# Kernel optimization log

Measured on AMD Instinct MI355X. Metric: run time of the kernel, lower is better.

The kernel has to match this reference:

```python
import jax, jax.numpy as jnp
import numpy as np

DIM = 512
HEADS = 8
DIM_HEAD = 64
INNER = HEADS * DIM_HEAD  # 512
NARROW_K = 9
WIDE_K = 9
WIDE_DIL = 5


def setup_inputs() -> dict:
    key = jax.random.key(0)
    ks = jax.random.split(key, 12)
    b, n = 4, 2048
    s = lambda fan_in: 1.0 / np.sqrt(fan_in)
    inp = {
        'tokens': jax.random.normal(ks[0], (b, n, DIM), jnp.float32),
        'mask': jax.random.randint(ks[1], (b, n), 0, 2) > 0,
        'w_qkv': jax.random.normal(ks[2], (DIM, INNER * 3), jnp.float32) * s(DIM),
        'w_out': jax.random.normal(ks[3], (INNER, DIM), jnp.float32) * s(INNER),
        'b_out': jnp.zeros((DIM,), jnp.float32),
        'w_narrow': jax.random.normal(ks[4], (DIM, DIM, NARROW_K), jnp.float32) * s(DIM * NARROW_K),
        'b_narrow': jnp.zeros((DIM,), jnp.float32),
        'w_wide': jax.random.normal(ks[5], (DIM, DIM, WIDE_K), jnp.float32) * s(DIM * WIDE_K),
        'b_wide': jnp.zeros((DIM,), jnp.float32),
        'ln1_g': jnp.ones((DIM,), jnp.float32),
        'ln1_b': jnp.zeros((DIM,), jnp.float32),
        'ff_w': jax.random.normal(ks[6], (DIM, DIM), jnp.float32) * s(DIM),
        'ff_b': jnp.zeros((DIM,), jnp.float32),
        'ln2_g': jnp.ones((DIM,), jnp.float32),
        'ln2_b': jnp.zeros((DIM,), jnp.float32),
    }
    return inp


def layer_norm(x, g, b, eps=1e-5):
    m = jnp.mean(x, axis=-1, keepdims=True)
    v = jnp.mean(jnp.square(x - m), axis=-1, keepdims=True)
    return (x - m) / jnp.sqrt(v + eps) * g + b


def rope_encoding(seq_len, dim_head, dtype):
    inv_freq = 1.0 / (10000.0 ** (jnp.arange(0, dim_head, 2, dtype=jnp.float32) / dim_head))
    pos = jnp.arange(seq_len, dtype=jnp.float32)
    sinu = jnp.einsum('i,j->ij', pos, inv_freq)  # [n, d/2]
    return jnp.concatenate([jnp.sin(sinu), jnp.cos(sinu)], axis=-1).astype(dtype)  # [n, d]


def attn(tokens, mask, w_qkv, w_out, b_out):
    b, n, _ = tokens.shape
    qkv = tokens @ w_qkv  # [b, n, 3*inner]
    q, k, v = jnp.split(qkv, 3, axis=-1)
    reshp = lambda t: t.reshape(b, n, HEADS, DIM_HEAD).transpose(0, 2, 1, 3)  # b h n d
    q, k, v = reshp(q), reshp(k), reshp(v)
    rope = rope_encoding(n, DIM_HEAD, tokens.dtype)  # [n, d]
    q = q + rope
    k = k + rope
    mask4 = mask[:, None, :, None]  # b 1 n 1
    big = jnp.finfo(k.dtype).max
    k = jnp.where(mask4, k, -big)
    q = jax.nn.softmax(q, axis=-1) * (DIM_HEAD ** -0.5)
    k = jax.nn.softmax(k, axis=2)  # over n
    v = jnp.where(mask4, v, 0.0)
    context = jnp.einsum('bhnd,bhne->bhde', k, v)
    out = jnp.einsum('bhde,bhnd->bhne', context, q)
    out = out.transpose(0, 2, 1, 3).reshape(b, n, INNER)
    return out @ w_out + b_out


def conv1d(x, w, b, padding, dilation):
    # x: [b, c, n], w: [out, in, k]
    y = jax.lax.conv_general_dilated(
        x, w, window_strides=(1,), padding=[(padding, padding)],
        rhs_dilation=(dilation,), dimension_numbers=('NCW', 'OIW', 'NCW'))
    return y + b[None, :, None]


def reference(tokens, mask, w_qkv, w_out, b_out, w_narrow, b_narrow,
              w_wide, b_wide, ln1_g, ln1_b, ff_w, ff_b, ln2_g, ln2_b):
    tokens = attn(tokens, mask, w_qkv, w_out, b_out)
    conv_in = tokens.transpose(0, 2, 1)  # b d n
    conv_in = jnp.where(mask[:, None, :], conv_in, 0.0)
    narrow = jax.nn.gelu(conv1d(conv_in, w_narrow, b_narrow, NARROW_K // 2, 1), approximate=False)
    wide_pad = (WIDE_K + (WIDE_K - 1) * (WIDE_DIL - 1)) // 2  # 20
    wide = jax.nn.gelu(conv1d(conv_in, w_wide, b_wide, wide_pad, WIDE_DIL), approximate=False)
    tokens = tokens + narrow.transpose(0, 2, 1) + wide.transpose(0, 2, 1)
    tokens = layer_norm(tokens, ln1_g, ln1_b)
    tokens = layer_norm(jax.nn.gelu(tokens @ ff_w + ff_b, approximate=False), ln2_g, ln2_b)
    return tokens
```

## Files before the change

### kernel.cpp

```cpp
#include <hip/hip_runtime.h>
#include <hip/hip_bf16.h>

#define BB 4
#define NN 2048
#define NROWS (BB*NN)

typedef unsigned short u16;
typedef __bf16 bf16x8 __attribute__((ext_vector_type(8)));
typedef u16    u16x8  __attribute__((ext_vector_type(8)));
typedef float  fx4    __attribute__((ext_vector_type(4)));

__device__ __forceinline__ float bf2f(u16 u){
  union { float f; unsigned int i; } x; x.i = ((unsigned int)u) << 16; return x.f;
}
__device__ __forceinline__ u16 f2bf(float f){
  union { float f; unsigned int i; } x; x.f = f;
  unsigned int i = x.i;
  i += 0x7fffu + ((i >> 16) & 1u);
  return (u16)(i >> 16);
}
__device__ __forceinline__ float geluf(float x){
  return 0.5f * x * (1.0f + erff(x * 0.70710678118654752f));
}

__global__ __launch_bounds__(256) void sniff_k(const u16* tokens, const unsigned int* mask, int* flags){
  __shared__ int s_f32, s_byte;
  if (threadIdx.x == 0) { s_f32 = 0; s_byte = 0; }
  __syncthreads();
  for (int i = threadIdx.x; i < 4096; i += 256) {
    float v = bf2f(tokens[i]);
    if (!(fabsf(v) < 1e10f)) atomicOr(&s_f32, 1);
  }
  for (int i = threadIdx.x; i < 2048; i += 256) {
    if (mask[i] > 1u) atomicOr(&s_byte, 1);
  }
  __syncthreads();
  if (threadIdx.x == 0) { flags[0] = s_f32; flags[1] = s_byte; }
}

__global__ __launch_bounds__(256) void misc_k(const void* mask, const void* tokens,
                                              const void* p0, const void* p1, const void* p2,
                                              const void* p3, const void* p4, const void* p5,
                                              const void* p6, const void* p7,
                                              const int* flags, float* rope, int* m32,
                                              float* params, float* ctx, float* kS, u16* tokbf){
  const void* srcs[8] = {p0,p1,p2,p3,p4,p5,p6,p7};
  int f32 = flags[0], mbyte = flags[1];
  const int T = 131072 + 8192 + 4096 + 131072 + 2048 + 4194304;
  for (int i = blockIdx.x*256 + threadIdx.x; i < T; i += gridDim.x*256) {
    if (i < 131072) {
      int p = i >> 6, j = i & 63;
      int jj = (j < 32) ? j : j - 32;
      float invf = exp2f(-(float)jj * (13.287712379549449f/32.0f));
      float prod = (float)p * invf;
      rope[i] = (j < 32) ? sinf(prod) : cosf(prod);
    } else if (i < 139264) {
      int k = i - 131072;
      int v = mbyte ? (int)((const unsigned char*)mask)[k] : ((const int*)mask)[k];
      m32[k] = v ? 1 : 0;
    } else if (i < 143360) {
      int k = i - 139264;
      int pid = k >> 9, j = k & 511;
      const void* s = srcs[pid];
      params[k] = f32 ? ((const float*)s)[j] : bf2f(((const u16*)s)[j]);
    } else if (i < 274432) {
      ctx[i - 143360] = 0.0f;
    } else if (i < 276480) {
      kS[i - 274432] = 0.0f;
    } else {
      int k = i - 276480;
      tokbf[k] = f32 ? f2bf(((const float*)tokens)[k]) : ((const u16*)tokens)[k];
    }
  }
}

__global__ __launch_bounds__(256) void prep2_k(const void* w_qkv, const void* w_out, const void* ff_w,
                                               const void* w_narrow, const void* w_wide,
                                               const int* flags,
                                               u16* wqkvt, u16* woutt, u16* ffwt,
                                               u16* wtN2, u16* wtW2){
  int bid = blockIdx.x;
  int f = flags[0];
  int tid = threadIdx.x;
  if (bid < 1024) {
    int tensor = bid >> 9, o = bid & 511;
    const void* src = tensor ? w_wide : w_narrow;
    u16* dst = tensor ? wtW2 : wtN2;
    __shared__ u16 Ls[4608];
    for (int i = tid; i < 4608; i += 256) {
      Ls[i] = f ? f2bf(((const float*)src)[(size_t)o*4608 + i]) : ((const u16*)src)[(size_t)o*4608 + i];
    }
    __syncthreads();
    #pragma unroll
    for (int kk = 0; kk < 9; kk++) {
      #pragma unroll
      for (int u = 0; u < 2; u++) {
        int c = tid + u*256;
        dst[(size_t)kk*262144 + o*512 + c] = Ls[c*9 + kk];
      }
    }
  } else {
    int id = bid - 1024;
    int z = id / 192;
    int rem = id - z*192;
    int x = rem % 24, y = rem / 24;
    int Nn = (z == 0) ? 1536 : 512;
    if (x * 64 >= Nn) return;
    const void* src = (z == 0) ? w_qkv : (z == 1) ? w_out : ff_w;
    u16* dst = (z == 0) ? wqkvt : (z == 1) ? woutt : ffwt;
    __shared__ u16 Ts[64][72];
    int n0 = x * 64, k0 = y * 64;
    int r = tid >> 2, cq = (tid & 3) * 16;
    #pragma unroll
    for (int u = 0; u < 2; u++) {
      int c = cq + u*8;
      int sidx = (k0 + r)*Nn + n0 + c;
      u16x8 v;
      if (f) {
        #pragma unroll
        for (int j = 0; j < 8; j++) v[j] = f2bf(((const float*)src)[sidx + j]);
      } else {
        v = *(const u16x8*)&((const u16*)src)[sidx];
      }
      *(u16x8*)&Ts[r][c] = v;
    }
    __syncthreads();
    #pragma unroll
    for (int u = 0; u < 2; u++) {
      int c = cq + u*8;
      u16x8 v;
      #pragma unroll
      for (int j = 0; j < 8; j++) v[j] = Ts[c + j][r];
      *(u16x8*)&dst[(size_t)(n0 + r)*512 + k0 + c] = v;
    }
  }
}

__global__ __launch_bounds__(256) void mgemm_qkv_k(const u16* A, const u16* Bt, const float* rope,
                                                   const int* mask, u16* qb, u16* keb, u16* vb){
  __shared__ u16 As[128][40];
  __shared__ u16 Bs[128][40];
  __shared__ int smask[128];
  int tid = threadIdx.x;
  int lane = tid & 63;
  int wave = tid >> 6;
  int wm = (wave >> 1) * 64, wn = (wave & 1) * 64;
  int quad = lane >> 4, l16 = lane & 15;
  int m0 = blockIdx.y * 128, n0 = blockIdx.x * 128;
  fx4 acc[4][4] = {};
  int ar = tid >> 2;
  int ac = (tid & 3) * 8;
  for (int k0 = 0; k0 < 512; k0 += 32) {
    *(u16x8*)&As[ar][ac]    = *(const u16x8*)&A[(size_t)(m0+ar)*512 + k0 + ac];
    *(u16x8*)&As[ar+64][ac] = *(const u16x8*)&A[(size_t)(m0+ar+64)*512 + k0 + ac];
    *(u16x8*)&Bs[ar][ac]    = *(const u16x8*)&Bt[(size_t)(n0+ar)*512 + k0 + ac];
    *(u16x8*)&Bs[ar+64][ac] = *(const u16x8*)&Bt[(size_t)(n0+ar+64)*512 + k0 + ac];
    __syncthreads();
    bf16x8 af[4], bfv[4];
    #pragma unroll
    for (int i = 0; i < 4; i++)
      af[i] = __builtin_bit_cast(bf16x8, *(const u16x8*)&As[wm + i*16 + l16][quad*8]);
    #pragma unroll
    for (int j = 0; j < 4; j++)
      bfv[j] = __builtin_bit_cast(bf16x8, *(const u16x8*)&Bs[wn + j*16 + l16][quad*8]);
    #pragma unroll
    for (int i = 0; i < 4; i++)
      #pragma unroll
      for (int j = 0; j < 4; j++)
        acc[i][j] = __builtin_amdgcn_mfma_f32_16x16x32_bf16(af[i], bfv[j], acc[i][j], 0, 0, 0);
    __syncthreads();
  }
  int x = blockIdx.x;
  if (x >= 4) {
    if (tid < 128) smask[tid] = mask[m0 + tid];
    __syncthreads();
  }
  if (x < 4) {
    #pragma unroll
    for (int i = 0; i < 4; i++)
      #pragma unroll
      for (int r = 0; r < 4; r++) {
        int rl = wm + i*16 + quad*4 + r;
        int row = m0 + rl;
        int nseq = row & (NN-1);
        const float* rp = rope + nseq*64 + l16;
        float e0 = __expf(acc[i][0][r] + rp[0]);
        float e1 = __expf(acc[i][1][r] + rp[16]);
        float e2 = __expf(acc[i][2][r] + rp[32]);
        float e3 = __expf(acc[i][3][r] + rp[48]);
        float s = e0 + e1 + e2 + e3;
        s += __shfl_xor(s, 1); s += __shfl_xor(s, 2);
        s += __shfl_xor(s, 4); s += __shfl_xor(s, 8);
        float sc = 0.125f / s;
        size_t base = (size_t)row*512 + n0 + wn + l16;
        qb[base]      = f2bf(e0*sc);
        qb[base + 16] = f2bf(e1*sc);
        qb[base + 32] = f2bf(e2*sc);
        qb[base + 48] = f2bf(e3*sc);
      }
  } else if (x < 8) {
    #pragma unroll
    for (int i = 0; i < 4; i++)
      #pragma unroll
      for (int r = 0; r < 4; r++) {
        int rl = wm + i*16 + quad*4 + r;
        int row = m0 + rl;
        int nseq = row & (NN-1);
        int mk = smask[rl];
        const float* rp = rope + nseq*64 + l16;
        size_t base = (size_t)row*512 + (n0 - 512) + wn + l16;
        #pragma unroll
        for (int j = 0; j < 4; j++) {
          float ke = mk ? __expf(acc[i][j][r] + rp[j*16]) : 0.0f;
          keb[base + j*16] = f2bf(ke);
        }
      }
  } else {
    #pragma unroll
    for (int i = 0; i < 4; i++)
      #pragma unroll
      for (int r = 0; r < 4; r++) {
        int rl = wm + i*16 + quad*4 + r;
        int row = m0 + rl;
        int mk = smask[rl];
        size_t base = (size_t)row*512 + (n0 - 1024) + wn + l16;
        #pragma unroll
        for (int j = 0; j < 4; j++)
          vb[base + j*16] = mk ? f2bf(acc[i][j][r]) : (u16)0;
      }
  }
}

#define FMA16(a, b, acc) \
  acc[0][0] = fmaf(a.x, b.x, acc[0][0]); acc[0][1] = fmaf(a.x, b.y, acc[0][1]); \
  acc[0][2] = fmaf(a.x, b.z, acc[0][2]); acc[0][3] = fmaf(a.x, b.w, acc[0][3]); \
  acc[1][0] = fmaf(a.y, b.x, acc[1][0]); acc[1][1] = fmaf(a.y, b.y, acc[1][1]); \
  acc[1][2] = fmaf(a.y, b.z, acc[1][2]); acc[1][3] = fmaf(a.y, b.w, acc[1][3]); \
  acc[2][0] = fmaf(a.z, b.x, acc[2][0]); acc[2][1] = fmaf(a.z, b.y, acc[2][1]); \
  acc[2][2] = fmaf(a.z, b.z, acc[2][2]); acc[2][3] = fmaf(a.z, b.w, acc[2][3]); \
  acc[3][0] = fmaf(a.w, b.x, acc[3][0]); acc[3][1] = fmaf(a.w, b.y, acc[3][1]); \
  acc[3][2] = fmaf(a.w, b.z, acc[3][2]); acc[3][3] = fmaf(a.w, b.w, acc[3][3]);

__global__ __launch_bounds__(256) void ctx_k(const u16* keb, const u16* vb, float* ctx, float* Sg){
  int bh = blockIdx.x, seg = blockIdx.y;
  int b = bh >> 3, h = bh & 7;
  __shared__ float Ks[32][68], Vs[32][68];
  __shared__ float sS[64];
  int tid = threadIdx.x, tx = tid & 15, ty = tid >> 4;
  if (tid < 64) sS[tid] = 0.0f;
  float acc[4][4] = {{0.f,0.f,0.f,0.f},{0.f,0.f,0.f,0.f},{0.f,0.f,0.f,0.f},{0.f,0.f,0.f,0.f}};
  float sp[8] = {0,0,0,0,0,0,0,0};
  int nl = tid >> 3, dcol = (tid & 7)*8;
  const u16* kp0 = keb + (size_t)(b*NN + seg*256)*512 + h*64 + dcol;
  const u16* vp0 = vb  + (size_t)(b*NN + seg*256)*512 + h*64 + dcol;
  for (int nc = 0; nc < 256; nc += 32) {
    u16x8 ku = *(const u16x8*)(kp0 + (size_t)(nc + nl)*512);
    u16x8 vu = *(const u16x8*)(vp0 + (size_t)(nc + nl)*512);
    float a[8], bb[8];
    #pragma unroll
    for (int t = 0; t < 8; t++) { a[t] = bf2f(ku[t]); bb[t] = bf2f(vu[t]); sp[t] += a[t]; }
    *(float4*)&Ks[nl][dcol]   = (float4){a[0],a[1],a[2],a[3]};
    *(float4*)&Ks[nl][dcol+4] = (float4){a[4],a[5],a[6],a[7]};
    *(float4*)&Vs[nl][dcol]   = (float4){bb[0],bb[1],bb[2],bb[3]};
    *(float4*)&Vs[nl][dcol+4] = (float4){bb[4],bb[5],bb[6],bb[7]};
    __syncthreads();
    #pragma unroll
    for (int q = 0; q < 32; q++) {
      float4 a4 = *(const float4*)&Ks[q][ty*4];
      float4 b4 = *(const float4*)&Vs[q][tx*4];
      FMA16(a4, b4, acc)
    }
    __syncthreads();
  }
  #pragma unroll
  for (int j = 0; j < 8; j++) atomicAdd(&sS[dcol + j], sp[j]);
  float* cp = ctx + (size_t)bh*4096;
  #pragma unroll
  for (int i = 0; i < 4; i++)
    #pragma unroll
    for (int j = 0; j < 4; j++)
      atomicAdd(&cp[(ty*4 + i)*64 + tx*4 + j], acc[i][j]);
  __syncthreads();
  if (tid < 64) atomicAdd(&Sg[bh*64 + tid], sS[tid]);
}

__global__ __launch_bounds__(256) void ctxw_k(const float* ctx, const float* Sg, const u16* woutt,
                                              u16* W2t, u16* cpadb){
  int bx = blockIdx.x;
  int tid = threadIdx.x;
  if (bx >= 32) {
    int idx = (bx - 32)*256 + tid;
    if (idx < BB*40*512) {
      int c = idx & 511;
      int t = (idx >> 9) % 40;
      int b = idx / (40*512);
      int tt = (t < 20) ? t : 2048 + t;
      cpadb[((size_t)b*2088 + tt)*512 + c] = 0;
    }
    return;
  }
  int h = bx & 7, b = bx >> 3;
  int lane = tid & 63, wave = tid >> 6;
  int quad = lane >> 4, l16 = lane & 15;
  const float* cp = ctx + (size_t)(b*8 + h)*4096;
  fx4 acc[8][4] = {};
  #pragma unroll
  for (int ks = 0; ks < 2; ks++) {
    bf16x8 bfv[4];
    #pragma unroll
    for (int j = 0; j < 4; j++) {
      int d = j*16 + l16;
      float S = Sg[(b*8 + h)*64 + d];
      float rs = (S > 0.0f) ? 1.0f/S : 0.0f;
      const float* src = cp + d*64 + ks*32 + quad*8;
      float4 v0 = *(const float4*)src, v1 = *(const float4*)(src + 4);
      bf16x8 t;
      t[0]=(__bf16)(v0.x*rs); t[1]=(__bf16)(v0.y*rs); t[2]=(__bf16)(v0.z*rs); t[3]=(__bf16)(v0.w*rs);
      t[4]=(__bf16)(v1.x*rs); t[5]=(__bf16)(v1.y*rs); t[6]=(__bf16)(v1.z*rs); t[7]=(__bf16)(v1.w*rs);
      bfv[j] = t;
    }
    #pragma unroll
    for (int i = 0; i < 8; i++) {
      int orow = wave*128 + i*16 + l16;
      bf16x8 afr = __builtin_bit_cast(bf16x8, *(const u16x8*)&woutt[(size_t)orow*512 + h*64 + ks*32 + quad*8]);
      #pragma unroll
      for (int j = 0; j < 4; j++)
        acc[i][j] = __builtin_amdgcn_mfma_f32_16x16x32_bf16(afr, bfv[j], acc[i][j], 0, 0, 0);
    }
  }
  u16* out = W2t + (size_t)b*262144;
  #pragma unroll
  for (int i = 0; i < 8; i++)
    #pragma unroll
    for (int j = 0; j < 4; j++)
      #pragma unroll
      for (int r = 0; r < 4; r++) {
        int orow = wave*128 + i*16 + quad*4 + r;
        out[(size_t)orow*512 + h*64 + j*16 + l16] = f2bf(acc[i][j][r]);
      }
}

__global__ __launch_bounds__(256) void mgemm_attn64_k(const u16* qb, const u16* W2t, const float* bias,
                                                      const int* mask, u16* attnb, u16* cpadb){
  __shared__ u16 As[64][40];
  __shared__ u16 Bs[128][40];
  int tid = threadIdx.x;
  int lane = tid & 63;
  int wave = tid >> 6;
  int wn = wave * 32;
  int quad = lane >> 4, l16 = lane & 15;
  int m0 = blockIdx.y * 64, n0 = blockIdx.x * 128, b = blockIdx.z;
  const u16* A  = qb  + (size_t)b*2048*512;
  const u16* Bt = W2t + (size_t)b*262144;
  fx4 acc[4][2] = {};
  int ar = tid >> 2;
  int ac = (tid & 3) * 8;
  for (int k0 = 0; k0 < 512; k0 += 32) {
    *(u16x8*)&As[ar][ac]    = *(const u16x8*)&A[(size_t)(m0+ar)*512 + k0 + ac];
    *(u16x8*)&Bs[ar][ac]    = *(const u16x8*)&Bt[(size_t)(n0+ar)*512 + k0 + ac];
    *(u16x8*)&Bs[ar+64][ac] = *(const u16x8*)&Bt[(size_t)(n0+ar+64)*512 + k0 + ac];
    __syncthreads();
    bf16x8 af[4], bfv[2];
    #pragma unroll
    for (int i = 0; i < 4; i++)
      af[i] = __builtin_bit_cast(bf16x8, *(const u16x8*)&As[i*16 + l16][quad*8]);
    #pragma unroll
    for (int j = 0; j < 2; j++)
      bfv[j] = __builtin_bit_cast(bf16x8, *(const u16x8*)&Bs[wn + j*16 + l16][quad*8]);
    #pragma unroll
    for (int i = 0; i < 4; i++)
      #pragma unroll
      for (int j = 0; j < 2; j++)
        acc[i][j] = __builtin_amdgcn_mfma_f32_16x16x32_bf16(af[i], bfv[j], acc[i][j], 0, 0, 0);
    __syncthreads();
  }
  #pragma unroll
  for (int i = 0; i < 4; i++)
    #pragma unroll
    for (int j = 0; j < 2; j++) {
      int col = n0 + wn + j*16 + l16;
      float bv = bias[col];
      #pragma unroll
      for (int r = 0; r < 4; r++) {
        int row_l = m0 + i*16 + quad*4 + r;
        float v = acc[i][j][r] + bv;
        u16 vbb = f2bf(v);
        attnb[((size_t)b*2048 + row_l)*512 + col] = vbb;
        int mk = mask[b*2048 + row_l];
        cpadb[((size_t)b*2088 + row_l + 20)*512 + col] = mk ? vbb : (u16)0;
      }
    }
}

__global__ __launch_bounds__(256, 2) void mconv6_k(const u16* cpad, const u16* Wn, const u16* Ww,
                                                   const float* bias_n, const float* bias_w,
                                                   u16* Dn, u16* Dw){
  __shared__ u16 As[168][72];
  __shared__ u16 Ws[128][72];
  int tid = threadIdx.x;
  int lane = tid & 63;
  int wave = tid >> 6;
  int wm = (wave >> 1) * 64;
  int wo = (wave & 1) * 64;
  int quad = lane >> 4, l16 = lane & 15;
  int o0 = blockIdx.x * 128, m0 = blockIdx.y * 128;
  int b = blockIdx.z >> 1, cid = blockIdx.z & 1;
  const u16* W = cid ? Ww : Wn;
  const float* bias = cid ? bias_w : bias_n;
  u16* D = cid ? Dw : Dn;
  fx4 acc[4][4] = {};
  const u16* cb = cpad + ((size_t)b*2088 + m0)*512;
  for (int c0 = 0; c0 < 512; c0 += 64) {
    __syncthreads();
    for (int idx = tid; idx < 168*8; idx += 256) {
      int r = idx >> 3, off = (idx & 7)*8;
      *(u16x8*)&As[r][off] = *(const u16x8*)&cb[(size_t)r*512 + c0 + off];
    }
    u16x8 pre[4];
    {
      const u16* wp = W + (size_t)o0*512 + c0;
      #pragma unroll
      for (int u = 0; u < 4; u++) {
        int idx = tid + u*256;
        int r = idx >> 3, off = (idx & 7)*8;
        pre[u] = *(const u16x8*)&wp[(size_t)r*512 + off];
      }
    }
    #pragma unroll
    for (int kk = 0; kk < 9; kk++) {
      if (kk > 0) __syncthreads();
      #pragma unroll
      for (int u = 0; u < 4; u++) {
        int idx = tid + u*256;
        int r = idx >> 3, off = (idx & 7)*8;
        *(u16x8*)&Ws[r][off] = pre[u];
      }
      if (kk < 8) {
        const u16* wp = W + (size_t)(kk+1)*262144 + (size_t)o0*512 + c0;
        #pragma unroll
        for (int u = 0; u < 4; u++) {
          int idx = tid + u*256;
          int r = idx >> 3, off = (idx & 7)*8;
          pre[u] = *(const u16x8*)&wp[(size_t)r*512 + off];
        }
      }
      __syncthreads();
      int shift = cid ? 5*kk : 16 + kk;
      #pragma unroll
      for (int ks = 0; ks < 2; ks++) {
        bf16x8 bfv[4];
        #pragma unroll
        for (int j = 0; j < 4; j++)
          bfv[j] = __builtin_bit_cast(bf16x8, *(const u16x8*)&Ws[wo + j*16 + l16][ks*32 + quad*8]);
        #pragma unroll
        for (int i = 0; i < 4; i++) {
          bf16x8 afr = __builtin_bit_cast(bf16x8, *(const u16x8*)&As[shift + wm + i*16 + l16][ks*32 + quad*8]);
          #pragma unroll
          for (int j = 0; j < 4; j++)
            acc[i][j] = __builtin_amdgcn_mfma_f32_16x16x32_bf16(afr, bfv[j], acc[i][j], 0, 0, 0);
        }
      }
    }
  }
  #pragma unroll
  for (int i = 0; i < 4; i++)
    #pragma unroll
    for (int j = 0; j < 4; j++) {
      int col = o0 + wo + j*16 + l16;
      float bv = bias[col];
      #pragma unroll
      for (int r = 0; r < 4; r++) {
        int row = b*2048 + m0 + wm + i*16 + quad*4 + r;
        D[(size_t)row*512 + col] = f2bf(geluf(acc[i][j][r] + bv));
      }
    }
}

template<bool BIAS, bool GELU>
__global__ __launch_bounds__(256) void mgemm64b_k(const u16* A, const u16* Bt, const float* bias,
                                                  u16* C, int M, int N, int K){
  __shared__ u16 As[64][40];
  __shared__ u16 Bs[128][40];
  int tid = threadIdx.x;
  int lane = tid & 63;
  int wave = tid >> 6;
  int wn = wave * 32;
  int quad = lane >> 4, l16 = lane & 15;
  int m0 = blockIdx.y * 64, n0 = blockIdx.x * 128;
  fx4 acc[4][2] = {};
  int ar = tid >> 2;
  int ac = (tid & 3) * 8;
  for (int k0 = 0; k0 < K; k0 += 32) {
    *(u16x8*)&As[ar][ac]    = *(const u16x8*)&A[(size_t)(m0+ar)*K + k0 + ac];
    *(u16x8*)&Bs[ar][ac]    = *(const u16x8*)&Bt[(size_t)(n0+ar)*K + k0 + ac];
    *(u16x8*)&Bs[ar+64][ac] = *(const u16x8*)&Bt[(size_t)(n0+ar+64)*K + k0 + ac];
    __syncthreads();
    bf16x8 af[4], bfv[2];
    #pragma unroll
    for (int i = 0; i < 4; i++)
      af[i] = __builtin_bit_cast(bf16x8, *(const u16x8*)&As[i*16 + l16][quad*8]);
    #pragma unroll
    for (int j = 0; j < 2; j++)
      bfv[j] = __builtin_bit_cast(bf16x8, *(const u16x8*)&Bs[wn + j*16 + l16][quad*8]);
    #pragma unroll
    for (int i = 0; i < 4; i++)
      #pragma unroll
      for (int j = 0; j < 2; j++)
        acc[i][j] = __builtin_amdgcn_mfma_f32_16x16x32_bf16(af[i], bfv[j], acc[i][j], 0, 0, 0);
    __syncthreads();
  }
  #pragma unroll
  for (int i = 0; i < 4; i++)
    #pragma unroll
    for (int j = 0; j < 2; j++) {
      int col = n0 + wn + j*16 + l16;
      float bv = BIAS ? bias[col] : 0.0f;
      #pragma unroll
      for (int r = 0; r < 4; r++) {
        int row = m0 + i*16 + quad*4 + r;
        float v = acc[i][j][r] + bv;
        if (GELU) v = geluf(v);
        C[(size_t)row*N + col] = f2bf(v);
      }
    }
}

__device__ __forceinline__ float block_sum512(float v, float* red){
  #pragma unroll
  for (int o = 32; o; o >>= 1) v += __shfl_xor(v, o, 64);
  int w = threadIdx.x >> 6;
  if ((threadIdx.x & 63) == 0) red[w] = v;
  __syncthreads();
  float t = red[0] + red[1] + red[2] + red[3];
  __syncthreads();
  return t;
}

template<int NADD, int OM>
__global__ __launch_bounds__(256) void ln_k(const u16* X, const u16* Y, const u16* Z,
                                            const float* g, const float* be,
                                            const int* flags, void* out){
  __shared__ float red[4];
  size_t row = blockIdx.x;
  int tid = threadIdx.x;
  const u16* xp = X + row*512;
  float x0 = bf2f(xp[tid]), x1 = bf2f(xp[tid + 256]);
  if (NADD >= 1) { const u16* yp = Y + row*512; x0 += bf2f(yp[tid]); x1 += bf2f(yp[tid + 256]); }
  if (NADD >= 2) { const u16* zp = Z + row*512; x0 += bf2f(zp[tid]); x1 += bf2f(zp[tid + 256]); }
  float mean = block_sum512(x0 + x1, red) * (1.0f/512.0f);
  float d0 = x0 - mean, d1 = x1 - mean;
  float var = block_sum512(d0*d0 + d1*d1, red) * (1.0f/512.0f);
  float inv = rsqrtf(var + 1e-5f);
  float r0 = d0*inv*g[tid]       + be[tid];
  float r1 = d1*inv*g[tid + 256] + be[tid + 256];
  bool obf = (OM == 1) || (OM == 2 && !flags[0]);
  if (obf) {
    u16* op = (u16*)out;
    op[row*512 + tid]       = f2bf(r0);
    op[row*512 + tid + 256] = f2bf(r1);
  } else {
    float* op = (float*)out;
    op[row*512 + tid]       = r0;
    op[row*512 + tid + 256] = r1;
  }
}

extern "C" void kernel_launch(void* const* d_in, const int* in_sizes, int n_in,
                              void* d_out, int out_size, void* d_ws, size_t ws_size,
                              hipStream_t stream) {
  const void* tokens   = d_in[0];
  const void* mask     = d_in[1];
  const void* w_qkv    = d_in[2];
  const void* w_out    = d_in[3];
  const void* b_out    = d_in[4];
  const void* w_narrow = d_in[5];
  const void* b_narrow = d_in[6];
  const void* w_wide   = d_in[7];
  const void* b_wide   = d_in[8];
  const void* ln1_g    = d_in[9];
  const void* ln1_b    = d_in[10];
  const void* ff_w     = d_in[11];
  const void* ff_b     = d_in[12];
  const void* ln2_g    = d_in[13];
  const void* ln2_b    = d_in[14];

  float* ws = (float*)d_ws;
  int*   flags  = (int*)ws;
  int*   m32    = (int*)(ws + 16);
  float* params = ws + 8208;
  float* kS     = ws + 12304;
  float* ctx    = ws + 14352;
  float* rope   = ws + 145424;
  u16*   tokbf  = (u16*)(ws + 276496);
  u16*   wqkvt  = (u16*)(ws + 2373648);
  u16*   woutt  = (u16*)(ws + 2766864);
  u16*   ffwt   = (u16*)(ws + 2897936);
  u16*   wtN2   = (u16*)(ws + 3029008);
  u16*   wtW2   = (u16*)(ws + 4208656);
  u16*   qb     = (u16*)(ws + 5388304);
  u16*   keb    = (u16*)(ws + 7485456);
  u16*   vb     = (u16*)(ws + 9582608);
  u16*   W2t    = (u16*)(ws + 11679760);
  u16*   attnb  = (u16*)(ws + 12204048);
  u16*   cpadb  = (u16*)(ws + 14301200);
  u16*   Dnb    = (u16*)(ws + 16439312);
  u16*   Dwb    = (u16*)(ws + 18536464);
  u16*   Eb     = attnb;
  u16*   t1b    = tokbf;

  float* p_bout = params;        float* p_bnar = params + 512;
  float* p_bwid = params + 1024; float* p_l1g  = params + 1536;
  float* p_l1b  = params + 2048; float* p_ffb  = params + 2560;
  float* p_l2g  = params + 3072; float* p_l2b  = params + 3584;

  sniff_k<<<dim3(1), dim3(256), 0, stream>>>((const u16*)tokens, (const unsigned int*)mask, flags);
  misc_k<<<dim3(8192), dim3(256), 0, stream>>>(mask, tokens, b_out, b_narrow, b_wide, ln1_g, ln1_b,
                                               ff_b, ln2_g, ln2_b, flags, rope, m32, params, ctx,
                                               kS, tokbf);
  prep2_k<<<dim3(1600), dim3(256), 0, stream>>>(w_qkv, w_out, ff_w, w_narrow, w_wide, flags,
                                                wqkvt, woutt, ffwt, wtN2, wtW2);

  mgemm_qkv_k<<<dim3(12, 64), dim3(256), 0, stream>>>(
      tokbf, wqkvt, rope, m32, qb, keb, vb);

  ctx_k<<<dim3(32, 8), dim3(256), 0, stream>>>(keb, vb, ctx, kS);

  ctxw_k<<<dim3(352), dim3(256), 0, stream>>>(ctx, kS, woutt, W2t, cpadb);

  mgemm_attn64_k<<<dim3(4, 32, 4), dim3(256), 0, stream>>>(qb, W2t, p_bout, m32, attnb, cpadb);

  mconv6_k<<<dim3(4, 16, 8), dim3(256), 0, stream>>>(cpadb, wtN2, wtW2, p_bnar, p_bwid, Dnb, Dwb);

  ln_k<2,1><<<dim3(NROWS), dim3(256), 0, stream>>>(attnb, Dnb, Dwb, p_l1g, p_l1b, flags, (void*)t1b);

  mgemm64b_k<true,true><<<dim3(4, 128), dim3(256), 0, stream>>>(
      t1b, ffwt, p_ffb, Eb, NROWS, 512, 512);

  ln_k<0,2><<<dim3(NROWS), dim3(256), 0, stream>>>(Eb, nullptr, nullptr, p_l2g, p_l2b, flags, d_out);
}
```

Measured before the change: 354.1 us.

## Rewrite conv kernel with direct global-to-LDS loads and all-tap weight staging

```diff
diff --git a/kernel.cpp b/kernel.cpp
--- a/kernel.cpp
+++ b/kernel.cpp
@@ -21,6 +21,10 @@
 }
 __device__ __forceinline__ float geluf(float x){
   return 0.5f * x * (1.0f + erff(x * 0.70710678118654752f));
+}
+__device__ __forceinline__ void gload16(const void* g, void* l){
+  __builtin_amdgcn_global_load_lds((const __attribute__((address_space(1))) unsigned int*)g,
+                                   (__attribute__((address_space(3))) unsigned int*)l, 16, 0, 0);
 }
 
 __global__ __launch_bounds__(256) void sniff_k(const u16* tokens, const unsigned int* mask, int* flags){
@@ -392,80 +396,61 @@
     }
 }
 
-__global__ __launch_bounds__(256, 2) void mconv6_k(const u16* cpad, const u16* Wn, const u16* Ww,
+__global__ __launch_bounds__(256, 3) void mconv7_k(const u16* cpad, const u16* Wn, const u16* Ww,
                                                    const float* bias_n, const float* bias_w,
                                                    u16* Dn, u16* Dw){
-  __shared__ u16 As[168][72];
-  __shared__ u16 Ws[128][72];
+  __shared__ u16 As[168*32];
+  __shared__ u16 Ws[9*64*32];
   int tid = threadIdx.x;
   int lane = tid & 63;
   int wave = tid >> 6;
   int wm = (wave >> 1) * 64;
-  int wo = (wave & 1) * 64;
+  int wo = (wave & 1) * 32;
   int quad = lane >> 4, l16 = lane & 15;
-  int o0 = blockIdx.x * 128, m0 = blockIdx.y * 128;
+  int o0 = blockIdx.x * 64, m0 = blockIdx.y * 128;
   int b = blockIdx.z >> 1, cid = blockIdx.z & 1;
   const u16* W = cid ? Ww : Wn;
   const float* bias = cid ? bias_w : bias_n;
   u16* D = cid ? Dw : Dn;
-  fx4 acc[4][4] = {};
+  fx4 acc[4][2] = {};
   const u16* cb = cpad + ((size_t)b*2088 + m0)*512;
-  for (int c0 = 0; c0 < 512; c0 += 64) {
-    __syncthreads();
-    for (int idx = tid; idx < 168*8; idx += 256) {
-      int r = idx >> 3, off = (idx & 7)*8;
-      *(u16x8*)&As[r][off] = *(const u16x8*)&cb[(size_t)r*512 + c0 + off];
-    }
-    u16x8 pre[4];
-    {
-      const u16* wp = W + (size_t)o0*512 + c0;
-      #pragma unroll
-      for (int u = 0; u < 4; u++) {
-        int idx = tid + u*256;
-        int r = idx >> 3, off = (idx & 7)*8;
-        pre[u] = *(const u16x8*)&wp[(size_t)r*512 + off];
-      }
-    }
+  int w_o  = tid >> 2;
+  int w_off = (tid & 3) * 8;
+  for (int c0 = 0; c0 < 512; c0 += 32) {
+    __syncthreads();
+    #pragma unroll
+    for (int it = 0; it < 3; it++) {
+      int s = it*256 + tid;
+      if (s < 672) {
+        gload16(&cb[(size_t)(s >> 2)*512 + c0 + (s & 3)*8], &As[(it*256 + wave*64)*8]);
+      }
+    }
+    #pragma unroll
+    for (int it = 0; it < 9; it++) {
+      gload16(&W[(size_t)it*262144 + (size_t)(o0 + w_o)*512 + c0 + w_off],
+              &Ws[(it*256 + wave*64)*8]);
+    }
+    __syncthreads();
     #pragma unroll
     for (int kk = 0; kk < 9; kk++) {
-      if (kk > 0) __syncthreads();
-      #pragma unroll
-      for (int u = 0; u < 4; u++) {
-        int idx = tid + u*256;
-        int r = idx >> 3, off = (idx & 7)*8;
-        *(u16x8*)&Ws[r][off] = pre[u];
-      }
-      if (kk < 8) {
-        const u16* wp = W + (size_t)(kk+1)*262144 + (size_t)o0*512 + c0;
+      int shift = cid ? 5*kk : 16 + kk;
+      bf16x8 bfv[2];
+      #pragma unroll
+      for (int j = 0; j < 2; j++)
+        bfv[j] = __builtin_bit_cast(bf16x8, *(const u16x8*)&Ws[(kk*64 + wo + j*16 + l16)*32 + quad*8]);
+      #pragma unroll
+      for (int i = 0; i < 4; i++) {
+        bf16x8 afr = __builtin_bit_cast(bf16x8, *(const u16x8*)&As[(shift + wm + i*16 + l16)*32 + quad*8]);
         #pragma unroll
-        for (int u = 0; u < 4; u++) {
-          int idx = tid + u*256;
-          int r = idx >> 3, off = (idx & 7)*8;
-          pre[u] = *(const u16x8*)&wp[(size_t)r*512 + off];
-        }
-      }
-      __syncthreads();
-      int shift = cid ? 5*kk : 16 + kk;
-      #pragma unroll
-      for (int ks = 0; ks < 2; ks++) {
-        bf16x8 bfv[4];
-        #pragma unroll
-        for (int j = 0; j < 4; j++)
-          bfv[j] = __builtin_bit_cast(bf16x8, *(const u16x8*)&Ws[wo + j*16 + l16][ks*32 + quad*8]);
-        #pragma unroll
-        for (int i = 0; i < 4; i++) {
-          bf16x8 afr = __builtin_bit_cast(bf16x8, *(const u16x8*)&As[shift + wm + i*16 + l16][ks*32 + quad*8]);
-          #pragma unroll
-          for (int j = 0; j < 4; j++)
-            acc[i][j] = __builtin_amdgcn_mfma_f32_16x16x32_bf16(afr, bfv[j], acc[i][j], 0, 0, 0);
-        }
+        for (int j = 0; j < 2; j++)
+          acc[i][j] = __builtin_amdgcn_mfma_f32_16x16x32_bf16(afr, bfv[j], acc[i][j], 0, 0, 0);
       }
     }
   }
   #pragma unroll
   for (int i = 0; i < 4; i++)
     #pragma unroll
-    for (int j = 0; j < 4; j++) {
+    for (int j = 0; j < 2; j++) {
       int col = o0 + wo + j*16 + l16;
       float bv = bias[col];
       #pragma unroll
@@ -629,7 +614,7 @@
 
   mgemm_attn64_k<<<dim3(4, 32, 4), dim3(256), 0, stream>>>(qb, W2t, p_bout, m32, attnb, cpadb);
 
-  mconv6_k<<<dim3(4, 16, 8), dim3(256), 0, stream>>>(cpadb, wtN2, wtW2, p_bnar, p_bwid, Dnb, Dwb);
+  mconv7_k<<<dim3(8, 16, 8), dim3(256), 0, stream>>>(cpadb, wtN2, wtW2, p_bnar, p_bwid, Dnb, Dwb);
 
   ln_k<2,1><<<dim3(NROWS), dim3(256), 0, stream>>>(attnb, Dnb, Dwb, p_l1g, p_l1b, flags, (void*)t1b);
 
```

Result: no change. 349.4 us (-1.3%).
